# Kernel tuning notes

Hardware: AMD Instinct MI355X
Metric: run time of the kernel (lower is better)

## Reference

```python
import jax, jax.numpy as jnp
import numpy as np

B, C1, C2, H, W = 16, 64, 64, 160, 160
K, KS, HID = 4, 3, 16  # K kernels, 3x3, hidden = max(int(64/16),16)=16
EPS = 1e-5


def setup_inputs() -> dict:
    key = jax.random.key(0)
    ks = jax.random.split(key, 8)
    fan_out = KS * KS * C2
    return {
        "x": jax.random.normal(ks[0], (B, C1, H, W), jnp.float32),
        # K candidate conv kernels and biases
        "Wk": jax.random.normal(ks[1], (K, C2, C1, KS, KS), jnp.float32) * np.sqrt(2.0 / fan_out),
        "bk": jnp.zeros((K, C2), jnp.float32),
        # attention trunk: 1x1 conv C1->HID (no bias), BN, ReLU
        "Wfc": jax.random.normal(ks[2], (HID, C1), jnp.float32) * 0.1,
        "gamma_h": jnp.ones((HID,), jnp.float32),
        "beta_h": jnp.zeros((HID,), jnp.float32),
        # four attention heads
        "Wf": jax.random.normal(ks[3], (C2, HID), jnp.float32) * 0.1,
        "bf": jnp.zeros((C2,), jnp.float32),
        "Ws": jax.random.normal(ks[4], (KS * KS, HID), jnp.float32) * 0.1,
        "bs": jnp.zeros((KS * KS,), jnp.float32),
        "Wc": jax.random.normal(ks[5], (C1, HID), jnp.float32) * 0.1,
        "bc": jnp.zeros((C1,), jnp.float32),
        "Ww": jax.random.normal(ks[6], (K, HID), jnp.float32) * 0.1,
        "bw": jnp.zeros((K,), jnp.float32),
        # outer BatchNorm2d params
        "gamma_o": jnp.ones((C2,), jnp.float32),
        "beta_o": jnp.zeros((C2,), jnp.float32),
    }


def reference(x, Wk, bk, Wfc, gamma_h, beta_h, Wf, bf, Ws, bs, Wc, bc, Ww, bw, gamma_o, beta_o):
    # ---- per-sample attention over K kernels ----
    ctx = x.mean(axis=(2, 3))                      # (B, C1)  global avg pool
    h = ctx @ Wfc.T                                # (B, HID) 1x1 conv == linear
    mu = h.mean(axis=0)
    var = h.var(axis=0)                            # biased, as torch BN training
    h = (h - mu) / jnp.sqrt(var + EPS) * gamma_h + beta_h
    h = jax.nn.relu(h)
    attn_f = jax.nn.sigmoid(h @ Wf.T + bf)         # (B, C2)
    attn_s = jax.nn.sigmoid(h @ Ws.T + bs).reshape(B, KS, KS)
    attn_c = jax.nn.sigmoid(h @ Wc.T + bc)         # (B, C1)
    attn_w = jax.nn.softmax(h @ Ww.T + bw, axis=-1)  # (B, K)

    # attn: (B, K, C2, C1, KS, KS) via broadcasting
    attn = (attn_w[:, :, None, None, None, None]
            * attn_f[:, None, :, None, None, None]
            * attn_c[:, None, None, :, None, None]
            * attn_s[:, None, None, None, :, :])
    weight = jnp.sum(attn * Wk[None], axis=1)      # (B, C2, C1, KS, KS)
    bias = attn_w @ bk                             # (B, C2)

    # ---- batched conv as grouped conv with groups=B ----
    out = jax.lax.conv_general_dilated(
        x.reshape(1, B * C1, H, W),
        weight.reshape(B * C2, C1, KS, KS),
        window_strides=(1, 1), padding=((1, 1), (1, 1)),
        dimension_numbers=('NCHW', 'OIHW', 'NCHW'),
        feature_group_count=B)                     # (1, B*C2, H, W)
    out = out.reshape(B, C2, H, W) + bias[:, :, None, None]

    # ---- outer BatchNorm2d (training stats) + SiLU ----
    mu_o = out.mean(axis=(0, 2, 3))
    var_o = out.var(axis=(0, 2, 3))
    out = (out - mu_o[None, :, None, None]) / jnp.sqrt(var_o + EPS)[None, :, None, None]
    out = out * gamma_o[None, :, None, None] + beta_o[None, :, None, None]
    return out * jax.nn.sigmoid(out)               # SiLU
```

## Files before the change

### kernel.cpp

```cpp
#include <hip/hip_runtime.h>
#include <math.h>

#define BB 16
#define C1 64
#define C2 64
#define HH 160
#define WW 160
#define KK 4
#define HID 16
#define EPS 1e-5f
#define HWSZ (HH*WW)
#define NPB (BB*HWSZ)

#define WS_AF    1024
#define WS_AC    2048
#define WS_AS    3072
#define WS_AW    3216
#define WS_BIAS  3280
#define WS_SC    4304
#define WS_SH    4368
#define WS_STATS 4432
#define NSLOT    32
#define WS_PART  8704
#define WS_ZERO  49664
#define WS_WEFF  50944
#define WS_XBF   345856

typedef __attribute__((ext_vector_type(8)))  short bf16x8;
typedef __attribute__((ext_vector_type(16))) float f32x16;

__device__ __forceinline__ unsigned short f2bf(float f) {
    unsigned int u = __float_as_uint(f);
    unsigned int r = (u + 0x7FFFu + ((u >> 16) & 1u)) >> 16;
    return (unsigned short)r;
}

__device__ __forceinline__ void gload16(const void* g, void* l) {
    __builtin_amdgcn_global_load_lds(
        (const __attribute__((address_space(1))) unsigned int*)g,
        (__attribute__((address_space(3))) unsigned int*)l, 16, 0, 0);
}

__global__ __launch_bounds__(256) void xprep_kernel(const float* __restrict__ x,
                                                    float* __restrict__ ws) {
    __shared__ float lds[10240];
    int bcc = blockIdx.y;
    int rg = blockIdx.x;
    int t = threadIdx.x;

    const float* src = x + (size_t)bcc * 16 * HWSZ + (size_t)rg * 4 * WW;
    float4* l4 = (float4*)lds;
    #pragma unroll
    for (int i = 0; i < 10; ++i) {
        int g = i * 256 + t;
        int ch = g / 160, rem = g - ch * 160;
        l4[g] = *(const float4*)(src + (size_t)ch * HWSZ + rem * 4);
    }
    __syncthreads();

    {
        int ch = t >> 4, j = t & 15;
        float s = 0.f;
        #pragma unroll
        for (int m = 0; m < 40; ++m) s += lds[ch * 640 + j + 16 * m];
        #pragma unroll
        for (int o = 8; o > 0; o >>= 1) s += __shfl_down(s, o, 16);
        if (j == 0) ws[WS_PART + ((size_t)bcc * 40 + rg) * 16 + ch] = s;
    }

    uint4* dst = (uint4*)(ws + WS_XBF) + ((size_t)bcc * 160 + rg * 4) * 320;
    #pragma unroll
    for (int i = 0; i < 5; ++i) {
        int u = i * 256 + t;
        int row = u / 320, rem = u - row * 320;
        int col = rem >> 1, p = rem & 1;
        int h = p ^ ((col >> 2) & 1) ^ 1;
        union { uint4 q; unsigned short us[8]; } pk;
        #pragma unroll
        for (int k = 0; k < 8; ++k)
            pk.us[k] = f2bf(lds[(h * 8 + k) * 640 + row * 160 + col]);
        dst[u] = pk.q;
    }
}

__global__ void attn_kernel(float* __restrict__ ws,
    const float* __restrict__ Wfc, const float* __restrict__ gh, const float* __restrict__ bh,
    const float* __restrict__ Wf,  const float* __restrict__ bf,
    const float* __restrict__ Wsm, const float* __restrict__ bs,
    const float* __restrict__ Wc,  const float* __restrict__ bc,
    const float* __restrict__ Ww,  const float* __restrict__ bw,
    const float* __restrict__ bk) {
    __shared__ float ctxs[16][64];
    __shared__ float hs[16][16];
    __shared__ float aw[16][4];
    int t = threadIdx.x;

    #pragma unroll
    for (int q = 0; q < 4; ++q) {
        int idx = t * 4 + q;
        int b = idx >> 6, c1 = idx & 63;
        const float* pp = ws + WS_PART + ((size_t)(b * 4 + (c1 >> 4)) * 40) * 16 + (c1 & 15);
        float s = 0.f;
        #pragma unroll
        for (int rg = 0; rg < 40; ++rg) s += pp[rg * 16];
        ctxs[b][c1] = s * (1.0f / (float)HWSZ);
    }
    __syncthreads();
    {
        int b = t >> 4, j = t & 15;
        const float* wr = Wfc + j * 64;
        float s = 0.f;
        #pragma unroll
        for (int c = 0; c < 64; c++) s += ctxs[b][c] * wr[c];
        hs[b][j] = s;
    }
    __syncthreads();
    if (t < 16) {
        int j = t;
        float mu = 0.f;
        #pragma unroll
        for (int b = 0; b < 16; b++) mu += hs[b][j];
        mu *= (1.f / 16.f);
        float vr = 0.f;
        #pragma unroll
        for (int b = 0; b < 16; b++) { float d = hs[b][j] - mu; vr += d * d; }
        vr *= (1.f / 16.f);
        float sc = gh[j] * rsqrtf(vr + EPS);
        float sh = bh[j] - mu * sc;
        #pragma unroll
        for (int b = 0; b < 16; b++) {
            float v = hs[b][j] * sc + sh;
            hs[b][j] = v > 0.f ? v : 0.f;
        }
    }
    __syncthreads();
    if (t < 16) {
        int b = t;
        float l[4]; float mx = -1e30f;
        #pragma unroll
        for (int k = 0; k < 4; k++) {
            float s = bw[k];
            #pragma unroll
            for (int j = 0; j < 16; j++) s += hs[b][j] * Ww[k * 16 + j];
            l[k] = s; mx = fmaxf(mx, s);
        }
        float den = 0.f;
        #pragma unroll
        for (int k = 0; k < 4; k++) { l[k] = expf(l[k] - mx); den += l[k]; }
        float r = 1.f / den;
        #pragma unroll
        for (int k = 0; k < 4; k++) { float v = l[k] * r; aw[b][k] = v; ws[WS_AW + b * 4 + k] = v; }
    }
    #pragma unroll
    for (int q = 0; q < 4; q++) {
        int idx = t * 4 + q;
        int b = idx >> 6, c2 = idx & 63;
        float sf = bf[c2], sc2 = bc[c2];
        #pragma unroll
        for (int j = 0; j < 16; j++) {
            float hv = hs[b][j];
            sf  += hv * Wf[c2 * 16 + j];
            sc2 += hv * Wc[c2 * 16 + j];
        }
        ws[WS_AF + idx] = 1.f / (1.f + expf(-sf));
        ws[WS_AC + idx] = 1.f / (1.f + expf(-sc2));
    }
    if (t < 144) {
        int b = t / 9, uv = t % 9;
        float s = bs[uv];
        #pragma unroll
        for (int j = 0; j < 16; j++) s += hs[b][j] * Wsm[uv * 16 + j];
        ws[WS_AS + t] = 1.f / (1.f + expf(-s));
    }
    __syncthreads();
    #pragma unroll
    for (int q = 0; q < 4; q++) {
        int idx = t * 4 + q;
        int b = idx >> 6, c2 = idx & 63;
        float s = 0.f;
        #pragma unroll
        for (int k = 0; k < 4; k++) s += aw[b][k] * bk[k * 64 + c2];
        ws[WS_BIAS + idx] = s;
    }
    for (int i = t; i < NSLOT * 128; i += 256) ws[WS_STATS + i] = 0.f;
}

__global__ void wprep_kernel(const float* __restrict__ Wk, float* __restrict__ ws) {
    int b = blockIdx.y;
    int tid = blockIdx.x * 256 + threadIdx.x;
    int h = tid & 1;
    int c2 = (tid >> 1) & 63;
    int g = tid >> 7;
    int uv = g % 9;
    int chunk = g / 9;
    const float* awp = ws + WS_AW + b * 4;
    float aw0 = awp[0], aw1 = awp[1], aw2 = awp[2], aw3 = awp[3];
    float af = ws[WS_AF + b * 64 + c2];
    float as_ = ws[WS_AS + b * 9 + uv];
    union { uint4 q; unsigned short u[8]; } pk;
    #pragma unroll
    for (int j = 0; j < 8; ++j) {
        int c1 = chunk * 16 + h * 8 + j;
        const float* wp = Wk + (size_t)(c2 * 64 + c1) * 9 + uv;
        float s = aw0 * wp[0] + aw1 * wp[64 * 64 * 9] + aw2 * wp[2 * 64 * 64 * 9] + aw3 * wp[3 * 64 * 64 * 9];
        float w = s * af * ws[WS_AC + b * 64 + c1] * as_;
        pk.u[j] = f2bf(w);
    }
    int unit = ((chunk * 9 + uv) * 64 + c2) * 2 + (h ^ ((c2 >> 2) & 1));
    ((uint4*)(ws + WS_WEFF))[(size_t)b * 4608 + unit] = pk.q;
}

__launch_bounds__(256, 2)
__global__ void conv_kernel(const float* __restrict__ wsf, float* __restrict__ out) {
    __shared__ uint4 xs[2][4 * 162 * 2];
    __shared__ uint4 wsh[1152];
    __shared__ float bsh[64];
    __shared__ float sst[128];

    int id = blockIdx.x;
    int b = id & 15;
    int bx = id >> 4;
    int y0 = bx * 2;
    int t = threadIdx.x;
    int wv = t >> 6;
    int lane = t & 63;
    int l31 = lane & 31;
    int l5 = lane >> 5;
    int c2h = wv & 1;
    int rw = wv >> 1;

    if (t < 64) bsh[t] = wsf[WS_BIAS + b * 64 + t];
    if (t >= 64 && t < 192) sst[t - 64] = 0.f;
    if (t >= 192 && t < 224) {
        int q = t - 192; int bq = q >> 4; q &= 15;
        int r = q >> 2, side = (q >> 1) & 1, p = q & 1;
        xs[bq][(r * 162 + side * 161) * 2 + p] = make_uint4(0, 0, 0, 0);
    }
    int rbad = (bx == 0) ? 0 : (bx == 79 ? 3 : -1);
    if (rbad >= 0) {
        for (int i = t; i < 640; i += 256)
            xs[i / 320][(rbad * 162 + 1) * 2 + (i % 320)] = make_uint4(0, 0, 0, 0);
    }

    const uint4* weff = (const uint4*)(wsf + WS_WEFF) + (size_t)b * 4608;
    const uint4* xbf  = (const uint4*)(wsf + WS_XBF);

    auto stage_x = [&](int cc, int bq) {
        for (int i = wv; i < 20; i += 4) {
            int r = i / 5, seg = i % 5;
            int gy = y0 - 1 + r;
            if (gy >= 0 && gy < HH)
                gload16(xbf + (((size_t)b * 4 + cc) * 160 + gy) * 320 + seg * 64 + lane,
                        (char*)&xs[bq][0] + ((r * 162 + 1) * 2 + seg * 64) * 16);
        }
    };
    auto stage_w = [&](int cc) {
        for (int i = wv; i < 18; i += 4)
            gload16(weff + (size_t)cc * 1152 + i * 64 + lane, (char*)wsh + i * 1024);
    };

    f32x16 acc[5];
    #pragma unroll
    for (int j = 0; j < 5; ++j)
        #pragma unroll
        for (int r = 0; r < 16; ++r) acc[j][r] = 0.f;

    stage_x(0, 0);
    stage_w(0);
    __syncthreads();

    int c2 = c2h * 32 + l31;
    int aswz = (l31 >> 2) & 1;
    int cur = 0;
    for (int cc = 0; cc < 4; ++cc) {
        if (cc < 3) stage_x(cc + 1, cur ^ 1);

        #pragma unroll
        for (int uv = 0; uv < 9; ++uv) {
            bf16x8 a = *(bf16x8*)&wsh[(uv * 64 + c2) * 2 + (l5 ^ aswz)];
            int xr = rw + uv / 3;
            int v = uv % 3;
            #pragma unroll
            for (int j = 0; j < 5; ++j) {
                int col = j * 32 + l31 + v;
                bf16x8 bb = *(bf16x8*)&xs[cur][(xr * 162 + col) * 2 + (l5 ^ (((col + 3) >> 2) & 1))];
                acc[j] = __builtin_amdgcn_mfma_f32_32x32x16_bf16(a, bb, acc[j], 0, 0, 0);
            }
        }
        asm volatile("s_waitcnt lgkmcnt(0)\n\ts_barrier" ::: "memory");
        if (cc < 3) {
            stage_w(cc + 1);
            asm volatile("s_waitcnt vmcnt(0) lgkmcnt(0)\n\ts_barrier" ::: "memory");
        }
        cur ^= 1;
    }

    float* outb = out + (size_t)b * C2 * HWSZ + (size_t)(y0 + rw) * WW;
    int cb = c2h * 32 + 4 * l5;
    float sr[16], qr[16];
    #pragma unroll
    for (int r = 0; r < 16; ++r) {
        int c2r = cb + (r & 3) + 8 * (r >> 2);
        float bias = bsh[c2r];
        float s = 0.f, q = 0.f;
        #pragma unroll
        for (int j = 0; j < 5; ++j) {
            float v = acc[j][r] + bias;
            outb[(size_t)c2r * HWSZ + j * 32 + l31] = v;
            s += v;
            q = fmaf(v, v, q);
        }
        sr[r] = s; qr[r] = q;
    }
    #pragma unroll
    for (int k = 0; k < 4; ++k) {
        int m = 1 << k, n = 8 >> k;
        #pragma unroll
        for (int i = 0; i < 8; ++i) {
            if (i < n) {
                float ks = (l31 & m) ? sr[i + n] : sr[i];
                float ss = (l31 & m) ? sr[i] : sr[i + n];
                sr[i] = ks + __shfl_xor(ss, m, 64);
                float kq = (l31 & m) ? qr[i + n] : qr[i];
                float sq = (l31 & m) ? qr[i] : qr[i + n];
                qr[i] = kq + __shfl_xor(sq, m, 64);
            }
        }
    }
    sr[0] += __shfl_xor(sr[0], 16, 64);
    qr[0] += __shfl_xor(qr[0], 16, 64);
    if (l31 < 16) {
        int rf = ((l31 & 1) << 3) | ((l31 & 2) << 1) | ((l31 & 4) >> 1) | ((l31 & 8) >> 3);
        int c2r = cb + (rf & 3) + 8 * (rf >> 2);
        atomicAdd(&sst[c2r], sr[0]);
        atomicAdd(&sst[64 + c2r], qr[0]);
    }
    __syncthreads();
    if (t < 128) {
        int slot = id & (NSLOT - 1);
        atomicAdd((float*)wsf + WS_STATS + slot * 128 + t, sst[t]);
    }
}

__global__ void bnact_kernel(float* __restrict__ out, const float* __restrict__ ws,
                             const float* __restrict__ go, const float* __restrict__ bo) {
    __shared__ float sc[64], sh[64];
    if (threadIdx.x < 64) {
        int c = threadIdx.x;
        float s = 0.f, q = 0.f;
        #pragma unroll
        for (int sl = 0; sl < NSLOT; sl++) {
            s += ws[WS_STATS + sl * 128 + c];
            q += ws[WS_STATS + sl * 128 + 64 + c];
        }
        float mu  = s * (1.0f / (float)NPB);
        float var = q * (1.0f / (float)NPB) - mu * mu;
        float scale = go[c] * rsqrtf(var + EPS);
        sc[c] = scale;
        sh[c] = bo[c] - mu * scale;
    }
    __syncthreads();
    const int n4 = BB * C2 * HWSZ / 4;
    for (int i = blockIdx.x * blockDim.x + threadIdx.x; i < n4; i += gridDim.x * blockDim.x) {
        float4 v = ((float4*)out)[i];
        int c = ((i * 4) / HWSZ) & 63;
        float s = sc[c], h = sh[c];
        v.x = v.x * s + h; v.y = v.y * s + h; v.z = v.z * s + h; v.w = v.w * s + h;
        v.x = v.x / (1.f + __expf(-v.x));
        v.y = v.y / (1.f + __expf(-v.y));
        v.z = v.z / (1.f + __expf(-v.z));
        v.w = v.w / (1.f + __expf(-v.w));
        ((float4*)out)[i] = v;
    }
}

extern "C" void kernel_launch(void* const* d_in, const int* in_sizes, int n_in,
                              void* d_out, int out_size, void* d_ws, size_t ws_size,
                              hipStream_t stream) {
    const float* x   = (const float*)d_in[0];
    const float* Wk  = (const float*)d_in[1];
    const float* bk  = (const float*)d_in[2];
    const float* Wfc = (const float*)d_in[3];
    const float* gh  = (const float*)d_in[4];
    const float* bh  = (const float*)d_in[5];
    const float* Wf  = (const float*)d_in[6];
    const float* bf  = (const float*)d_in[7];
    const float* Wsm = (const float*)d_in[8];
    const float* bs  = (const float*)d_in[9];
    const float* Wc  = (const float*)d_in[10];
    const float* bc  = (const float*)d_in[11];
    const float* Ww  = (const float*)d_in[12];
    const float* bw  = (const float*)d_in[13];
    const float* go  = (const float*)d_in[14];
    const float* bo  = (const float*)d_in[15];
    float* out = (float*)d_out;
    float* ws  = (float*)d_ws;

    xprep_kernel<<<dim3(40, 64), dim3(256), 0, stream>>>(x, ws);
    attn_kernel<<<dim3(1), dim3(256), 0, stream>>>(ws, Wfc, gh, bh, Wf, bf, Wsm, bs, Wc, bc, Ww, bw, bk);
    wprep_kernel<<<dim3(18, 16), dim3(256), 0, stream>>>(Wk, ws);
    conv_kernel<<<dim3(1280), dim3(256), 0, stream>>>(ws, out);
    bnact_kernel<<<dim3(2048), dim3(256), 0, stream>>>(out, ws, go, bo);
}
```

Before: 137.9 us.

## Drop LDS staging in conv; load MFMA operands directly from global memory

The conv kernel stops staging the bf16 input rows and effective weights through double-buffered LDS. MFMA operands are now read straight from global memory, relying on L1/L2 caches, and padding is handled by pointing out-of-range rows and columns at a zeroed workspace region. This removes LDS traffic and block barriers, and allows raising the occupancy hint from 2 to 4 blocks per CU. The cost is more global and cache load traffic with no explicit reuse, plus added latency exposure.

```diff
diff --git a/kernel.cpp b/kernel.cpp
--- a/kernel.cpp
+++ b/kernel.cpp
@@ -17,14 +17,12 @@
 #define WS_AS    3072
 #define WS_AW    3216
 #define WS_BIAS  3280
-#define WS_SC    4304
-#define WS_SH    4368
 #define WS_STATS 4432
 #define NSLOT    32
 #define WS_PART  8704
 #define WS_ZERO  49664
-#define WS_WEFF  50944
-#define WS_XBF   345856
+#define WS_WEFF  53760
+#define WS_XBF   348672
 
 typedef __attribute__((ext_vector_type(8)))  short bf16x8;
 typedef __attribute__((ext_vector_type(16))) float f32x16;
@@ -33,12 +31,6 @@
     unsigned int u = __float_as_uint(f);
     unsigned int r = (u + 0x7FFFu + ((u >> 16) & 1u)) >> 16;
     return (unsigned short)r;
-}
-
-__device__ __forceinline__ void gload16(const void* g, void* l) {
-    __builtin_amdgcn_global_load_lds(
-        (const __attribute__((address_space(1))) unsigned int*)g,
-        (__attribute__((address_space(3))) unsigned int*)l, 16, 0, 0);
 }
 
 __global__ __launch_bounds__(256) void xprep_kernel(const float* __restrict__ x,
@@ -183,6 +175,7 @@
         ws[WS_BIAS + idx] = s;
     }
     for (int i = t; i < NSLOT * 128; i += 256) ws[WS_STATS + i] = 0.f;
+    for (int i = t; i < 4096; i += 256) ws[WS_ZERO + i] = 0.f;
 }
 
 __global__ void wprep_kernel(const float* __restrict__ Wk, float* __restrict__ ws) {
@@ -210,11 +203,8 @@
     ((uint4*)(ws + WS_WEFF))[(size_t)b * 4608 + unit] = pk.q;
 }
 
-__launch_bounds__(256, 2)
+__launch_bounds__(256, 4)
 __global__ void conv_kernel(const float* __restrict__ wsf, float* __restrict__ out) {
-    __shared__ uint4 xs[2][4 * 162 * 2];
-    __shared__ uint4 wsh[1152];
-    __shared__ float bsh[64];
     __shared__ float sst[128];
 
     int id = blockIdx.x;
@@ -229,35 +219,20 @@
     int c2h = wv & 1;
     int rw = wv >> 1;
 
-    if (t < 64) bsh[t] = wsf[WS_BIAS + b * 64 + t];
-    if (t >= 64 && t < 192) sst[t - 64] = 0.f;
-    if (t >= 192 && t < 224) {
-        int q = t - 192; int bq = q >> 4; q &= 15;
-        int r = q >> 2, side = (q >> 1) & 1, p = q & 1;
-        xs[bq][(r * 162 + side * 161) * 2 + p] = make_uint4(0, 0, 0, 0);
-    }
-    int rbad = (bx == 0) ? 0 : (bx == 79 ? 3 : -1);
-    if (rbad >= 0) {
-        for (int i = t; i < 640; i += 256)
-            xs[i / 320][(rbad * 162 + 1) * 2 + (i % 320)] = make_uint4(0, 0, 0, 0);
-    }
-
-    const uint4* weff = (const uint4*)(wsf + WS_WEFF) + (size_t)b * 4608;
-    const uint4* xbf  = (const uint4*)(wsf + WS_XBF);
-
-    auto stage_x = [&](int cc, int bq) {
-        for (int i = wv; i < 20; i += 4) {
-            int r = i / 5, seg = i % 5;
-            int gy = y0 - 1 + r;
-            if (gy >= 0 && gy < HH)
-                gload16(xbf + (((size_t)b * 4 + cc) * 160 + gy) * 320 + seg * 64 + lane,
-                        (char*)&xs[bq][0] + ((r * 162 + 1) * 2 + seg * 64) * 16);
-        }
-    };
-    auto stage_w = [&](int cc) {
-        for (int i = wv; i < 18; i += 4)
-            gload16(weff + (size_t)cc * 1152 + i * 64 + lane, (char*)wsh + i * 1024);
-    };
+    if (t < 128) sst[t] = 0.f;
+
+    const char* xb    = (const char*)(wsf + WS_XBF) + (size_t)b * 4 * 819200;
+    const char* weffb = (const char*)(wsf + WS_WEFF) + (size_t)b * 73728;
+    const char* zp    = (const char*)(wsf + WS_ZERO) + 64;
+
+    int c2 = c2h * 32 + l31;
+    int a_off = (c2 * 2 + (l5 ^ ((c2 >> 2) & 1))) * 16;
+    int boff[3];
+    #pragma unroll
+    for (int v = 0; v < 3; ++v) {
+        int gxv = l31 + v - 1;
+        boff[v] = gxv * 32 + ((l5 ^ (gxv >> 2) ^ 1) & 1) * 16;
+    }
 
     f32x16 acc[5];
     #pragma unroll
@@ -265,34 +240,31 @@
         #pragma unroll
         for (int r = 0; r < 16; ++r) acc[j][r] = 0.f;
 
-    stage_x(0, 0);
-    stage_w(0);
-    __syncthreads();
-
-    int c2 = c2h * 32 + l31;
-    int aswz = (l31 >> 2) & 1;
-    int cur = 0;
     for (int cc = 0; cc < 4; ++cc) {
-        if (cc < 3) stage_x(cc + 1, cur ^ 1);
-
-        #pragma unroll
-        for (int uv = 0; uv < 9; ++uv) {
-            bf16x8 a = *(bf16x8*)&wsh[(uv * 64 + c2) * 2 + (l5 ^ aswz)];
-            int xr = rw + uv / 3;
-            int v = uv % 3;
+        const char* wrow = weffb + cc * 18432;
+        const char* xcc  = xb + (size_t)cc * 819200;
+        #pragma unroll
+        for (int u = 0; u < 3; ++u) {
+            int gy = y0 + rw - 1 + u;
+            const char* rb = (gy >= 0 && gy < HH) ? xcc + gy * 5120 : zp;
             #pragma unroll
-            for (int j = 0; j < 5; ++j) {
-                int col = j * 32 + l31 + v;
-                bf16x8 bb = *(bf16x8*)&xs[cur][(xr * 162 + col) * 2 + (l5 ^ (((col + 3) >> 2) & 1))];
-                acc[j] = __builtin_amdgcn_mfma_f32_32x32x16_bf16(a, bb, acc[j], 0, 0, 0);
+            for (int v = 0; v < 3; ++v) {
+                bf16x8 a = *(const bf16x8*)(wrow + (u * 3 + v) * 2048 + a_off);
+                const char* bp = rb + boff[v];
+                const char* bp0 = (v == 0 && l31 == 0)  ? zp : bp;
+                const char* bp4 = (v == 2 && l31 == 31) ? zp : bp;
+                bf16x8 b0 = *(const bf16x8*)(bp0);
+                bf16x8 b1 = *(const bf16x8*)(bp + 1024);
+                bf16x8 b2 = *(const bf16x8*)(bp + 2048);
+                bf16x8 b3 = *(const bf16x8*)(bp + 3072);
+                bf16x8 b4 = *(const bf16x8*)(bp4 + 4096);
+                acc[0] = __builtin_amdgcn_mfma_f32_32x32x16_bf16(a, b0, acc[0], 0, 0, 0);
+                acc[1] = __builtin_amdgcn_mfma_f32_32x32x16_bf16(a, b1, acc[1], 0, 0, 0);
+                acc[2] = __builtin_amdgcn_mfma_f32_32x32x16_bf16(a, b2, acc[2], 0, 0, 0);
+                acc[3] = __builtin_amdgcn_mfma_f32_32x32x16_bf16(a, b3, acc[3], 0, 0, 0);
+                acc[4] = __builtin_amdgcn_mfma_f32_32x32x16_bf16(a, b4, acc[4], 0, 0, 0);
             }
         }
-        asm volatile("s_waitcnt lgkmcnt(0)\n\ts_barrier" ::: "memory");
-        if (cc < 3) {
-            stage_w(cc + 1);
-            asm volatile("s_waitcnt vmcnt(0) lgkmcnt(0)\n\ts_barrier" ::: "memory");
-        }
-        cur ^= 1;
     }
 
     float* outb = out + (size_t)b * C2 * HWSZ + (size_t)(y0 + rw) * WW;
@@ -301,7 +273,7 @@
     #pragma unroll
     for (int r = 0; r < 16; ++r) {
         int c2r = cb + (r & 3) + 8 * (r >> 2);
-        float bias = bsh[c2r];
+        float bias = wsf[WS_BIAS + b * 64 + c2r];
         float s = 0.f, q = 0.f;
         #pragma unroll
         for (int j = 0; j < 5; ++j) {
@@ -329,6 +301,7 @@
     }
     sr[0] += __shfl_xor(sr[0], 16, 64);
     qr[0] += __shfl_xor(qr[0], 16, 64);
+    __syncthreads();
     if (l31 < 16) {
         int rf = ((l31 & 1) << 3) | ((l31 & 2) << 1) | ((l31 & 4) >> 1) | ((l31 & 8) >> 3);
         int c2r = cb + (rf & 3) + 8 * (rf >> 2);
```

Result: slower. 165.1 us (+19.7%).
